# Optimization experiments

Measured on AMD Instinct MI355X. Metric: run time of the kernel, lower is better.

Reference implementation:

```python
import math
import jax, jax.numpy as jnp
import numpy as np

B, C, E = 8, 2048, 1024

def setup_inputs() -> dict:
    key = jax.random.key(0)
    ks = jax.random.split(key, 7)
    s_e = 1.0 / math.sqrt(E)
    s_c = 1.0 / math.sqrt(C)
    return {
        'x': jax.random.normal(ks[0], (B, C, E), dtype=jnp.float32),
        'fc_w': jax.random.normal(ks[1], (E, E), dtype=jnp.float32) * s_e,
        'fc_b': jax.random.normal(ks[2], (E,), dtype=jnp.float32) * s_e,
        'alt_fc_w': jax.random.normal(ks[3], (C, C), dtype=jnp.float32) * s_c,
        'alt_fc_b': jax.random.normal(ks[4], (C,), dtype=jnp.float32) * s_c,
        'vfc_w': jax.random.normal(ks[5], (E, E), dtype=jnp.float32) * s_e,
        'vfc_b': jax.random.normal(ks[6], (E,), dtype=jnp.float32) * s_e,
    }

def reference(x, fc_w, fc_b, alt_fc_w, alt_fc_b, vfc_w, vfc_b):
    # y = fc(x): [b,c,e]
    y = jnp.einsum('bce,fe->bcf', x, fc_w) + fc_b
    # yx = alt_fc(x^T): [b,e,c] -> Linear over context dim -> [b,e,k]
    xx = jnp.swapaxes(x, 1, 2)                    # [b,e,c]
    yx = jnp.einsum('bec,kc->bek', xx, alt_fc_w) + alt_fc_b
    # attention scores: [b,c,k]
    attn = jnp.einsum('bce,bek->bck', y, yx)
    scale = 1.0 / math.sqrt(attn.shape[-1])
    attn = jax.nn.softmax(attn * scale, axis=-1)
    # values
    vx = jnp.einsum('bke,fe->bkf', x, vfc_w) + vfc_b
    out = jnp.einsum('bck,bke->bce', attn, vx)
    # post_feed=None -> return y only
    return out
```

## Files before the change

### kernel.cpp

```cpp
#include <hip/hip_runtime.h>
#include <stdint.h>

#define Bb 8
#define Cc 2048
#define Ee 1024

typedef unsigned short u16;
typedef __attribute__((ext_vector_type(8))) short short8;
typedef __attribute__((ext_vector_type(4))) float f32x4;

__device__ __forceinline__ u16 f2bf(float f){
    unsigned u = __builtin_bit_cast(unsigned, f);
    return (u16)((u + 0x7fffu + ((u >> 16) & 1u)) >> 16);
}
__device__ __forceinline__ float bf2f(u16 h){
    return __builtin_bit_cast(float, ((unsigned)h) << 16);
}
__device__ __forceinline__ void gld16(const void* g, void* l){
    __builtin_amdgcn_global_load_lds(
        (const __attribute__((address_space(1))) unsigned int*)g,
        (__attribute__((address_space(3))) unsigned int*)l,
        16, 0, 0);
}
#define MFMA(a,b,c) __builtin_amdgcn_mfma_f32_16x16x32_bf16((a),(b),(c),0,0,0)
#define SBAR()  __builtin_amdgcn_s_barrier()
#define SCHED0() __builtin_amdgcn_sched_barrier(0)
#define LGKM0() asm volatile("s_waitcnt lgkmcnt(0)" ::: "memory")
#define VMCNT6() asm volatile("s_waitcnt vmcnt(6)" ::: "memory")
#define VMCNT2() asm volatile("s_waitcnt vmcnt(2)" ::: "memory")
#define VMCNT0() asm volatile("s_waitcnt vmcnt(0)" ::: "memory")

__global__ __launch_bounds__(256) void k_cast(const float* __restrict__ s,
                                              u16* __restrict__ d, long n4){
    long i = (long)blockIdx.x * 256 + threadIdx.x;
    const long stride = (long)gridDim.x * 256;
    for (; i < n4; i += stride){
        float4 f = ((const float4*)s)[i];
        ushort4 o = make_ushort4(f2bf(f.x), f2bf(f.y), f2bf(f.z), f2bf(f.w));
        ((ushort4*)d)[i] = o;
    }
}

__global__ __launch_bounds__(256) void k_cast_xt(const float* __restrict__ src,
                                                 u16* __restrict__ xb,
                                                 u16* __restrict__ xbT){
    __shared__ float tile[32][33];
    const int b = blockIdx.z;
    src += (long)b * Cc * Ee;
    xb  += (long)b * Cc * Ee;
    xbT += (long)b * Cc * Ee;
    const int c0 = blockIdx.x * 32;
    const int r0 = blockIdx.y * 32;
    const int tx = threadIdx.x & 31;
    const int ty = threadIdx.x >> 5;
    #pragma unroll
    for (int p = 0; p < 4; ++p){
        float v = src[(long)(r0 + ty + p*8) * Ee + c0 + tx];
        tile[ty + p*8][tx] = v;
        xb[(long)(r0 + ty + p*8) * Ee + c0 + tx] = f2bf(v);
    }
    __syncthreads();
    #pragma unroll
    for (int p = 0; p < 4; ++p)
        xbT[(long)(c0 + ty + p*8) * Cc + r0 + tx] = f2bf(tile[tx][ty + p*8]);
}

template<int BIAS_MODE, int OUT_F32>
__global__ __launch_bounds__(512, 2)
void k_gemm256(const u16* __restrict__ A, const u16* __restrict__ Bm,
               void* __restrict__ Cout, const float* __restrict__ bias,
               int N, int K, long sA, long sB, long sC, float scale)
{
    __shared__ __attribute__((aligned(16))) char smem[131072];

    const int gx = gridDim.x, gy = gridDim.y;
    const int nwg = gx * gy * gridDim.z;
    const int lin = blockIdx.x + gx * (blockIdx.y + gy * blockIdx.z);
    const int swz = (lin & 7) * (nwg >> 3) + (lin >> 3);
    const int bx = swz % gx;
    const int tmp = swz / gx;
    const int by = tmp % gy;
    const int bz = tmp / gy;

    A  += (long)bz * sA;
    Bm += (long)bz * sB;
    u16*   Cm = (u16*)Cout + (OUT_F32 ? 0 : (long)bz * sC);
    float* Cf = (float*)Cout + (OUT_F32 ? (long)bz * sC : 0);

    const int tid  = threadIdx.x;
    const int lane = tid & 63;
    const int wave = tid >> 6;
    const int wr = wave >> 2;
    const int wc = wave & 3;
    const int tileM = bx * 256;
    const int tileN = by * 256;

    const int srow   = tid >> 3;
    const int schunk = (tid & 7) ^ (srow & 7);
    const u16* Ag = A  + (long)(tileM + srow) * K + schunk * 8;
    const u16* Bg = Bm + (long)(tileN + srow) * K + schunk * 8;
    const long uK = (long)64 * K;
    const int  ldst = tid * 16;

    const int lrow = lane & 15;
    const int lk   = lane >> 4;
    const int sw   = lrow & 7;
    const int cs0  = ((0 + lk) ^ sw) * 16;
    const int cs1  = ((4 + lk) ^ sw) * 16;
    const int arow0 = (wr*128 + lrow) * 128;
    const int brow0 = 32768 + (wc*64 + lrow) * 128;

    f32x4 acc[8][4];
    #pragma unroll
    for (int m = 0; m < 8; ++m)
        #pragma unroll
        for (int n = 0; n < 4; ++n)
            acc[m][n] = (f32x4){0.f,0.f,0.f,0.f};

    char* sm = smem;
    #pragma unroll
    for (int u = 0; u < 4; ++u) gld16(Bg + u*uK, sm + 32768 + u*8192 + ldst);
    #pragma unroll
    for (int u = 0; u < 4; ++u) gld16(Ag + u*uK, sm + u*8192 + ldst);
    __syncthreads();

    const int NT = K >> 6;
    short8 aF[4], bK0[4], bK1[4];

    for (int t = 0; t < NT; ++t){
        const bool pref = (t + 1) < NT;
        char* cbuf = sm + ((t & 1) << 16);
        char* nbuf = sm + (((t + 1) & 1) << 16);
        const u16* Agt = Ag + (long)(t + 1) * 64;
        const u16* Bgt = Bg + (long)(t + 1) * 64;

        #pragma unroll
        for (int m = 0; m < 4; ++m) aF[m]  = *(const short8*)(cbuf + arow0 + m*2048 + cs0);
        #pragma unroll
        for (int n = 0; n < 4; ++n) bK0[n] = *(const short8*)(cbuf + brow0 + n*2048 + cs0);
        if (pref){ gld16(Agt + 0*uK, nbuf + 0*8192 + ldst);
                   gld16(Agt + 2*uK, nbuf + 2*8192 + ldst);
                   gld16(Bgt + 0*uK, nbuf + 32768 + 0*8192 + ldst);
                   gld16(Bgt + 1*uK, nbuf + 32768 + 1*8192 + ldst); }
        SCHED0(); SBAR(); LGKM0(); SCHED0();
        __builtin_amdgcn_s_setprio(1);
        #pragma unroll
        for (int m = 0; m < 4; ++m)
            #pragma unroll
            for (int n = 0; n < 4; ++n)
                acc[m][n] = MFMA(aF[m], bK0[n], acc[m][n]);
        __builtin_amdgcn_s_setprio(0);
        SBAR(); SCHED0();

        #pragma unroll
        for (int m = 0; m < 4; ++m) aF[m]  = *(const short8*)(cbuf + arow0 + m*2048 + cs1);
        #pragma unroll
        for (int n = 0; n < 4; ++n) bK1[n] = *(const short8*)(cbuf + brow0 + n*2048 + cs1);
        if (pref){ gld16(Bgt + 2*uK, nbuf + 32768 + 2*8192 + ldst);
                   gld16(Bgt + 3*uK, nbuf + 32768 + 3*8192 + ldst); }
        SCHED0(); SBAR(); LGKM0(); SCHED0();
        __builtin_amdgcn_s_setprio(1);
        #pragma unroll
        for (int m = 0; m < 4; ++m)
            #pragma unroll
            for (int n = 0; n < 4; ++n)
                acc[m][n] = MFMA(aF[m], bK1[n], acc[m][n]);
        __builtin_amdgcn_s_setprio(0);
        if (pref){ VMCNT6(); } else { VMCNT0(); }
        SBAR(); SCHED0();

        #pragma unroll
        for (int m = 0; m < 4; ++m) aF[m] = *(const short8*)(cbuf + arow0 + (m+4)*2048 + cs0);
        SCHED0(); SBAR(); LGKM0(); SCHED0();
        __builtin_amdgcn_s_setprio(1);
        #pragma unroll
        for (int m = 0; m < 4; ++m)
            #pragma unroll
            for (int n = 0; n < 4; ++n)
                acc[m+4][n] = MFMA(aF[m], bK0[n], acc[m+4][n]);
        __builtin_amdgcn_s_setprio(0);
        SBAR(); SCHED0();

        #pragma unroll
        for (int m = 0; m < 4; ++m) aF[m] = *(const short8*)(cbuf + arow0 + (m+4)*2048 + cs1);
        if (pref){ gld16(Agt + 1*uK, nbuf + 1*8192 + ldst);
                   gld16(Agt + 3*uK, nbuf + 3*8192 + ldst); }
        SCHED0(); SBAR(); LGKM0(); SCHED0();
        __builtin_amdgcn_s_setprio(1);
        #pragma unroll
        for (int m = 0; m < 4; ++m)
            #pragma unroll
            for (int n = 0; n < 4; ++n)
                acc[m+4][n] = MFMA(aF[m], bK1[n], acc[m+4][n]);
        __builtin_amdgcn_s_setprio(0);
        if (pref){ VMCNT2(); }
        SBAR(); SCHED0();
    }

    const int r0base = tileM + wr*128 + lk*4;
    const int cbase  = tileN + wc*64 + lrow;
    #pragma unroll
    for (int m = 0; m < 8; ++m){
        const int r0 = r0base + m*16;
        #pragma unroll
        for (int n = 0; n < 4; ++n){
            const int c = cbase + n*16;
            f32x4 v = acc[m][n];
            #pragma unroll
            for (int j = 0; j < 4; ++j){
                float val = v[j] * scale;
                if (BIAS_MODE == 1) val += bias[c];
                if (BIAS_MODE == 2) val += bias[r0 + j];
                if (OUT_F32) Cf[(long)(r0 + j) * N + c] = val;
                else         Cm[(long)(r0 + j) * N + c] = f2bf(val);
            }
        }
    }
}

__global__ __launch_bounds__(256) void k_softmax(u16* __restrict__ P){
    u16* p = P + (long)blockIdx.x * Cc;
    const int tid = threadIdx.x;
    short8 raw = *(const short8*)(p + tid * 8);
    float v[8];
    float mx = -3.0e38f;
    #pragma unroll
    for (int i = 0; i < 8; ++i){ v[i] = bf2f((u16)raw[i]); mx = fmaxf(mx, v[i]); }
    #pragma unroll
    for (int o = 32; o > 0; o >>= 1) mx = fmaxf(mx, __shfl_xor(mx, o));
    __shared__ float redm[4];
    if ((tid & 63) == 0) redm[tid >> 6] = mx;
    __syncthreads();
    mx = fmaxf(fmaxf(redm[0], redm[1]), fmaxf(redm[2], redm[3]));
    float s = 0.f;
    #pragma unroll
    for (int i = 0; i < 8; ++i){ v[i] = __expf(v[i] - mx); s += v[i]; }
    #pragma unroll
    for (int o = 32; o > 0; o >>= 1) s += __shfl_xor(s, o);
    __shared__ float reds[4];
    if ((tid & 63) == 0) reds[tid >> 6] = s;
    __syncthreads();
    s = reds[0] + reds[1] + reds[2] + reds[3];
    const float inv = 1.f / s;
    short8 o8;
    #pragma unroll
    for (int i = 0; i < 8; ++i) o8[i] = (short)f2bf(v[i] * inv);
    *(short8*)(p + tid * 8) = o8;
}

static inline int cast_grid(long n4){
    long g = (n4 + 255) / 256;
    return (int)(g > 2048 ? 2048 : g);
}

extern "C" void kernel_launch(void* const* d_in, const int* in_sizes, int n_in,
                              void* d_out, int out_size, void* d_ws, size_t ws_size,
                              hipStream_t stream)
{
    const float* x     = (const float*)d_in[0];
    const float* fc_w  = (const float*)d_in[1];
    const float* fc_b  = (const float*)d_in[2];
    const float* altw  = (const float*)d_in[3];
    const float* altb  = (const float*)d_in[4];
    const float* vfc_w = (const float*)d_in[5];
    const float* vfc_b = (const float*)d_in[6];
    float* out = (float*)d_out;

    char* ws = (char*)d_ws;
    const size_t nBCE = (size_t)Bb * Cc * Ee;
    u16* xb   = (u16*)(ws);
    u16* xbT  = (u16*)(ws + 2 * nBCE);
    u16* P    = (u16*)(ws);
    u16* y    = (u16*)(ws + 4 * nBCE);
    u16* z    = (u16*)(ws + 6 * nBCE);
    u16* vxT  = (u16*)(ws + 8 * nBCE);
    u16* fcwb = (u16*)(ws + 10 * nBCE);
    u16* vfwb = fcwb + (size_t)Ee * Ee;
    u16* awb  = vfwb + (size_t)Ee * Ee;

    k_cast_xt<<<dim3(Ee / 32, Cc / 32, Bb), 256, 0, stream>>>(x, xb, xbT);
    k_cast<<<cast_grid((long)Ee * Ee / 4), 256, 0, stream>>>(fc_w, fcwb, (long)Ee * Ee / 4);
    k_cast<<<cast_grid((long)Ee * Ee / 4), 256, 0, stream>>>(vfc_w, vfwb, (long)Ee * Ee / 4);
    k_cast<<<cast_grid((long)Cc * Cc / 4), 256, 0, stream>>>(altw, awb, (long)Cc * Cc / 4);

    const long sBCE = (long)Cc * Ee;
    const long sBCC = (long)Cc * Cc;
    dim3 blk(512);

    k_gemm256<1, 0><<<dim3(Cc/256, Ee/256, Bb), blk, 0, stream>>>(
        xb, fcwb, y, fc_b, Ee, Ee, sBCE, 0, sBCE, 1.f);

    k_gemm256<2, 0><<<dim3(Ee/256, Cc/256, Bb), blk, 0, stream>>>(
        vfwb, xb, vxT, vfc_b, Cc, Ee, 0, sBCE, sBCE, 1.f);

    k_gemm256<2, 0><<<dim3(Cc/256, Ee/256, Bb), blk, 0, stream>>>(
        awb, xbT, z, altb, Ee, Cc, 0, sBCE, sBCE, 1.f);

    k_gemm256<0, 0><<<dim3(Cc/256, Cc/256, Bb), blk, 0, stream>>>(
        y, z, P, nullptr, Cc, Ee, sBCE, sBCE, sBCC, 0.022097086912079608f);

    k_softmax<<<Bb * Cc, 256, 0, stream>>>(P);

    k_gemm256<0, 1><<<dim3(Cc/256, Ee/256, Bb), blk, 0, stream>>>(
        P, vxT, out, nullptr, Ee, Cc, sBCC, sBCE, sBCE, 1.f);
}
```

Measured before the change: 348.9 us.

## Restructure GEMM main loop with one barrier per K-tile and register double-buffering

Reworks the bf16 MFMA GEMM inner loop. All eight global-to-LDS prefetches for the next tile are now issued at the start of each iteration. A second A fragment register set lets LDS reads for the next sub-step overlap with MFMAs, gated by partial lgkmcnt waits. The four per-iteration barrier pairs collapse into one vmcnt(0)+barrier at the end, cutting synchronisation stalls at the cost of more registers and a full wait on the prefetch each iteration.

```diff
diff --git a/kernel.cpp b/kernel.cpp
--- a/kernel.cpp
+++ b/kernel.cpp
@@ -25,9 +25,9 @@
 #define MFMA(a,b,c) __builtin_amdgcn_mfma_f32_16x16x32_bf16((a),(b),(c),0,0,0)
 #define SBAR()  __builtin_amdgcn_s_barrier()
 #define SCHED0() __builtin_amdgcn_sched_barrier(0)
+#define LGKM8() asm volatile("s_waitcnt lgkmcnt(8)" ::: "memory")
+#define LGKM4() asm volatile("s_waitcnt lgkmcnt(4)" ::: "memory")
 #define LGKM0() asm volatile("s_waitcnt lgkmcnt(0)" ::: "memory")
-#define VMCNT6() asm volatile("s_waitcnt vmcnt(6)" ::: "memory")
-#define VMCNT2() asm volatile("s_waitcnt vmcnt(2)" ::: "memory")
 #define VMCNT0() asm volatile("s_waitcnt vmcnt(0)" ::: "memory")
 
 __global__ __launch_bounds__(256) void k_cast(const float* __restrict__ s,
@@ -125,7 +125,7 @@
     __syncthreads();
 
     const int NT = K >> 6;
-    short8 aF[4], bK0[4], bK1[4];
+    short8 aA[4], aB[4], bK0[4], bK1[4];
 
     for (int t = 0; t < NT; ++t){
         const bool pref = (t + 1) < NT;
@@ -134,67 +134,67 @@
         const u16* Agt = Ag + (long)(t + 1) * 64;
         const u16* Bgt = Bg + (long)(t + 1) * 64;
 
-        #pragma unroll
-        for (int m = 0; m < 4; ++m) aF[m]  = *(const short8*)(cbuf + arow0 + m*2048 + cs0);
+        if (pref){
+            gld16(Agt + 0*uK, nbuf + 0*8192 + ldst);
+            gld16(Agt + 1*uK, nbuf + 1*8192 + ldst);
+            gld16(Agt + 2*uK, nbuf + 2*8192 + ldst);
+            gld16(Agt + 3*uK, nbuf + 3*8192 + ldst);
+            gld16(Bgt + 0*uK, nbuf + 32768 + 0*8192 + ldst);
+            gld16(Bgt + 1*uK, nbuf + 32768 + 1*8192 + ldst);
+            gld16(Bgt + 2*uK, nbuf + 32768 + 2*8192 + ldst);
+            gld16(Bgt + 3*uK, nbuf + 32768 + 3*8192 + ldst);
+        }
+
+        #pragma unroll
+        for (int m = 0; m < 4; ++m) aA[m]  = *(const short8*)(cbuf + arow0 + m*2048 + cs0);
         #pragma unroll
         for (int n = 0; n < 4; ++n) bK0[n] = *(const short8*)(cbuf + brow0 + n*2048 + cs0);
-        if (pref){ gld16(Agt + 0*uK, nbuf + 0*8192 + ldst);
-                   gld16(Agt + 2*uK, nbuf + 2*8192 + ldst);
-                   gld16(Bgt + 0*uK, nbuf + 32768 + 0*8192 + ldst);
-                   gld16(Bgt + 1*uK, nbuf + 32768 + 1*8192 + ldst); }
-        SCHED0(); SBAR(); LGKM0(); SCHED0();
+        #pragma unroll
+        for (int m = 0; m < 4; ++m) aB[m]  = *(const short8*)(cbuf + arow0 + m*2048 + cs1);
+        #pragma unroll
+        for (int n = 0; n < 4; ++n) bK1[n] = *(const short8*)(cbuf + brow0 + n*2048 + cs1);
+
+        LGKM8(); SCHED0();
         __builtin_amdgcn_s_setprio(1);
         #pragma unroll
         for (int m = 0; m < 4; ++m)
             #pragma unroll
             for (int n = 0; n < 4; ++n)
-                acc[m][n] = MFMA(aF[m], bK0[n], acc[m][n]);
+                acc[m][n] = MFMA(aA[m], bK0[n], acc[m][n]);
         __builtin_amdgcn_s_setprio(0);
-        SBAR(); SCHED0();
-
-        #pragma unroll
-        for (int m = 0; m < 4; ++m) aF[m]  = *(const short8*)(cbuf + arow0 + m*2048 + cs1);
-        #pragma unroll
-        for (int n = 0; n < 4; ++n) bK1[n] = *(const short8*)(cbuf + brow0 + n*2048 + cs1);
-        if (pref){ gld16(Bgt + 2*uK, nbuf + 32768 + 2*8192 + ldst);
-                   gld16(Bgt + 3*uK, nbuf + 32768 + 3*8192 + ldst); }
-        SCHED0(); SBAR(); LGKM0(); SCHED0();
+
+        #pragma unroll
+        for (int m = 0; m < 4; ++m) aA[m] = *(const short8*)(cbuf + arow0 + (m+4)*2048 + cs0);
+        LGKM4(); SCHED0();
         __builtin_amdgcn_s_setprio(1);
         #pragma unroll
         for (int m = 0; m < 4; ++m)
             #pragma unroll
             for (int n = 0; n < 4; ++n)
-                acc[m][n] = MFMA(aF[m], bK1[n], acc[m][n]);
+                acc[m][n] = MFMA(aB[m], bK1[n], acc[m][n]);
         __builtin_amdgcn_s_setprio(0);
-        if (pref){ VMCNT6(); } else { VMCNT0(); }
-        SBAR(); SCHED0();
-
-        #pragma unroll
-        for (int m = 0; m < 4; ++m) aF[m] = *(const short8*)(cbuf + arow0 + (m+4)*2048 + cs0);
-        SCHED0(); SBAR(); LGKM0(); SCHED0();
+
+        #pragma unroll
+        for (int m = 0; m < 4; ++m) aB[m] = *(const short8*)(cbuf + arow0 + (m+4)*2048 + cs1);
+        LGKM4(); SCHED0();
         __builtin_amdgcn_s_setprio(1);
         #pragma unroll
         for (int m = 0; m < 4; ++m)
             #pragma unroll
             for (int n = 0; n < 4; ++n)
-                acc[m+4][n] = MFMA(aF[m], bK0[n], acc[m+4][n]);
+                acc[m+4][n] = MFMA(aA[m], bK0[n], acc[m+4][n]);
         __builtin_amdgcn_s_setprio(0);
-        SBAR(); SCHED0();
-
-        #pragma unroll
-        for (int m = 0; m < 4; ++m) aF[m] = *(const short8*)(cbuf + arow0 + (m+4)*2048 + cs1);
-        if (pref){ gld16(Agt + 1*uK, nbuf + 1*8192 + ldst);
-                   gld16(Agt + 3*uK, nbuf + 3*8192 + ldst); }
-        SCHED0(); SBAR(); LGKM0(); SCHED0();
+
+        LGKM0(); SCHED0();
         __builtin_amdgcn_s_setprio(1);
         #pragma unroll
         for (int m = 0; m < 4; ++m)
             #pragma unroll
             for (int n = 0; n < 4; ++n)
-                acc[m+4][n] = MFMA(aF[m], bK1[n], acc[m+4][n]);
+                acc[m+4][n] = MFMA(aB[m], bK1[n], acc[m+4][n]);
         __builtin_amdgcn_s_setprio(0);
-        if (pref){ VMCNT2(); }
-        SBAR(); SCHED0();
+
+        VMCNT0(); SBAR(); SCHED0();
     }
 
     const int r0base = tileM + wr*128 + lk*4;
```

Result: faster. 340.6 us (-2.4%).
